# Optimization experiments

Hardware: AMD Instinct MI355X
Metric: run time of the kernel (lower is better)

## Reference

```python
import jax, jax.numpy as jnp
import numpy as np

DIM = 512
NUM_HEADS = 8
HEAD_DIM = DIM // NUM_HEADS
SCALE = HEAD_DIM ** -0.5


def setup_inputs() -> dict:
    key = jax.random.key(0)
    k1, k2, k3, k4 = jax.random.split(key, 4)
    B, C, H, W = 2, DIM, 64, 64
    x = jax.random.normal(k1, (B, C, H, W), dtype=jnp.float32)
    # torch Linear weights are [out, in]; init ~ U(-1/sqrt(in), 1/sqrt(in))
    lim = 1.0 / np.sqrt(C)
    w_qkv = jax.random.uniform(k2, (3 * C, C), minval=-lim, maxval=lim, dtype=jnp.float32)
    w_proj = jax.random.uniform(k3, (C, C), minval=-lim, maxval=lim, dtype=jnp.float32)
    b_proj = jax.random.uniform(k4, (C,), minval=-lim, maxval=lim, dtype=jnp.float32)
    return {"x": x, "w_qkv": w_qkv, "w_proj": w_proj, "b_proj": b_proj}


def reference(x, w_qkv, w_proj, b_proj):
    B, C, H, W = x.shape
    N = H * W
    h, hd = NUM_HEADS, C // NUM_HEADS
    # (B,C,H,W) -> (B,N,C)
    tokens = jnp.transpose(x, (0, 2, 3, 1)).reshape(B, N, C)
    qkv = tokens @ w_qkv.T                              # (B,N,3C)
    qkv = qkv.reshape(B, N, 3, h, hd)
    qkv = jnp.transpose(qkv, (2, 0, 3, 1, 4))           # (3,B,h,N,hd)
    q, k, v = qkv[0], qkv[1], qkv[2]
    k = k * SCALE
    # role-swapped attention: softmax over (k v^T) then apply to q
    attn = jax.nn.softmax(jnp.einsum('bhnd,bhmd->bhnm', k, v), axis=-1)  # (B,h,N,N)
    out = jnp.einsum('bhnm,bhmd->bhnd', attn, q)        # (B,h,N,hd)
    out = jnp.transpose(out, (0, 2, 1, 3)).reshape(B, H, W, C)
    # faithful to original: permute back to (B,C,H,W) THEN reshape to (B,N,C)
    out = jnp.transpose(out, (0, 3, 1, 2)).reshape(B, N, C)
    out = out @ w_proj.T + b_proj
    return out.reshape(B, C, H, W)
```

## Files before the change

kernel.cpp:

```cpp
#include <hip/hip_runtime.h>
#include <hip/hip_bf16.h>
#include <cstdint>


typedef __bf16 bf16_t;
typedef __bf16 bf16x8 __attribute__((ext_vector_type(8)));
typedef float f32x4 __attribute__((ext_vector_type(4)));
typedef unsigned int u32x4 __attribute__((ext_vector_type(4)));

#define DEVFN static __device__ __forceinline__
#define LOG2E 1.4426950408889634f

DEVFN f32x4 mfma16(bf16x8 a, bf16x8 b, f32x4 c) {
  return __builtin_amdgcn_mfma_f32_16x16x32_bf16(a, b, c, 0, 0, 0);
}
DEVFN unsigned bfbits(float x) { return (unsigned)__builtin_bit_cast(unsigned short, (bf16_t)x); }
DEVFN unsigned pack2(float lo, float hi) { return bfbits(lo) | (bfbits(hi) << 16); }

__global__ __launch_bounds__(256) void k_transpose_x(const float* __restrict__ x,
                                                     bf16_t* __restrict__ xT) {
  __shared__ bf16_t tile[64][72];
  int bid = blockIdx.x;
  int ntile = bid & 63;
  int ctile = (bid >> 6) & 7;
  int b = bid >> 9;
  int n0 = ntile << 6, c0 = ctile << 6;
  int t = threadIdx.x;
  int ci = t >> 2, nc = (t & 3) << 4;
  const float4* src4 = reinterpret_cast<const float4*>(
      x + (size_t)(b * 512 + c0 + ci) * 4096 + n0 + nc);
#pragma unroll
  for (int j4 = 0; j4 < 4; ++j4) {
    float4 v = src4[j4];
    tile[ci][nc + j4 * 4 + 0] = (bf16_t)v.x;
    tile[ci][nc + j4 * 4 + 1] = (bf16_t)v.y;
    tile[ci][nc + j4 * 4 + 2] = (bf16_t)v.z;
    tile[ci][nc + j4 * 4 + 3] = (bf16_t)v.w;
  }
  __syncthreads();
  int ni = t & 63, cc = (t >> 6) << 4;
  unsigned ob[8];
#pragma unroll
  for (int j = 0; j < 8; ++j) {
    unsigned lo = (unsigned)__builtin_bit_cast(unsigned short, tile[cc + 2 * j][ni]);
    unsigned hi = (unsigned)__builtin_bit_cast(unsigned short, tile[cc + 2 * j + 1][ni]);
    ob[j] = lo | (hi << 16);
  }
  bf16_t* dst = xT + (size_t)(b * 4096 + n0 + ni) * 512 + c0 + cc;
  reinterpret_cast<u32x4*>(dst)[0] = *(u32x4*)&ob[0];
  reinterpret_cast<u32x4*>(dst)[1] = *(u32x4*)&ob[4];
}

__global__ __launch_bounds__(256) void k_convert_w(const float* __restrict__ w,
                                                   bf16_t* __restrict__ o, int do_scale) {
  int i = (blockIdx.x * 256 + threadIdx.x) * 4;
  float4 v = *reinterpret_cast<const float4*>(w + i);
  if (do_scale) {
    const float s = 0.125f * LOG2E;
    int m = i >> 9;
    if (m >= 512 && m < 1024) { v.x *= s; v.y *= s; v.z *= s; v.w *= s; }
  }
  uint2 st; st.x = pack2(v.x, v.y); st.y = pack2(v.z, v.w);
  *reinterpret_cast<uint2*>(o + i) = st;
}

__global__ __launch_bounds__(512, 4) void k_qkv_gemm(const bf16_t* __restrict__ xT,
                                                     const bf16_t* __restrict__ wq,
                                                     bf16_t* __restrict__ Qn,
                                                     bf16_t* __restrict__ Katt,
                                                     bf16_t* __restrict__ Vbuf) {
  __shared__ bf16_t As[2][128 * 64];
  __shared__ bf16_t Bs[2][128 * 64];
  int bid = blockIdx.x;
  int tm = bid / 12, tn = bid % 12;
  int tid = threadIdx.x;
  int lane = tid & 63, wave = tid >> 6;
  int n15 = lane & 15, g = lane >> 4;
  int wm = wave & 1, wn = wave >> 1;
  int row0 = tm * 128, col0 = tn * 128;

  int srow = tid >> 3, sslot = tid & 7;
  int sgran = sslot ^ (srow & 7);
  const bf16_t* Ag = xT + (size_t)(row0 + srow) * 512 + sgran * 8;
  const bf16_t* Bg = wq + (size_t)(col0 + srow) * 512 + sgran * 8;
  int sdst = srow * 64 + sslot * 8;

  u32x4 ra0 = *reinterpret_cast<const u32x4*>(Ag);
  u32x4 ra1 = *reinterpret_cast<const u32x4*>(Ag + 64 * 512);
  u32x4 rb0 = *reinterpret_cast<const u32x4*>(Bg);
  u32x4 rb1 = *reinterpret_cast<const u32x4*>(Bg + 64 * 512);
  *reinterpret_cast<u32x4*>(&As[0][sdst]) = ra0;
  *reinterpret_cast<u32x4*>(&As[0][sdst + 4096]) = ra1;
  *reinterpret_cast<u32x4*>(&Bs[0][sdst]) = rb0;
  *reinterpret_cast<u32x4*>(&Bs[0][sdst + 4096]) = rb1;
  __syncthreads();

  f32x4 acc[4][2] = {};
  int cur = 0;
  for (int step = 0; step < 8; ++step) {
    if (step < 7) {
      int k0n = (step + 1) << 6;
      ra0 = *reinterpret_cast<const u32x4*>(Ag + k0n);
      ra1 = *reinterpret_cast<const u32x4*>(Ag + 64 * 512 + k0n);
      rb0 = *reinterpret_cast<const u32x4*>(Bg + k0n);
      rb1 = *reinterpret_cast<const u32x4*>(Bg + 64 * 512 + k0n);
    }
    const bf16_t* Al = As[cur];
    const bf16_t* Bl = Bs[cur];
#pragma unroll
    for (int kh = 0; kh < 2; ++kh) {
      bf16x8 a[4], b[2];
#pragma unroll
      for (int mf = 0; mf < 4; ++mf) {
        int r = wm * 64 + mf * 16 + n15;
        a[mf] = *reinterpret_cast<const bf16x8*>(Al + r * 64 + (((kh * 4 + g) ^ (r & 7)) << 3));
      }
#pragma unroll
      for (int nf = 0; nf < 2; ++nf) {
        int r = wn * 32 + nf * 16 + n15;
        b[nf] = *reinterpret_cast<const bf16x8*>(Bl + r * 64 + (((kh * 4 + g) ^ (r & 7)) << 3));
      }
#pragma unroll
      for (int mf = 0; mf < 4; ++mf)
#pragma unroll
        for (int nf = 0; nf < 2; ++nf) acc[mf][nf] = mfma16(a[mf], b[nf], acc[mf][nf]);
    }
    if (step < 7) {
      *reinterpret_cast<u32x4*>(&As[cur ^ 1][sdst]) = ra0;
      *reinterpret_cast<u32x4*>(&As[cur ^ 1][sdst + 4096]) = ra1;
      *reinterpret_cast<u32x4*>(&Bs[cur ^ 1][sdst]) = rb0;
      *reinterpret_cast<u32x4*>(&Bs[cur ^ 1][sdst + 4096]) = rb1;
    }
    __syncthreads();
    cur ^= 1;
  }
  int t = col0 >> 9;
  bf16_t* dstbuf = (t == 0) ? Qn : (t == 1) ? Katt : Vbuf;
#pragma unroll
  for (int mf = 0; mf < 4; ++mf)
#pragma unroll
    for (int r = 0; r < 4; ++r) {
      int rgl = row0 + wm * 64 + mf * 16 + g * 4 + r;
      int b_ = rgl >> 12, n = rgl & 4095;
#pragma unroll
      for (int nf = 0; nf < 2; ++nf) {
        int col = col0 + wn * 32 + nf * 16 + n15;
        int h = (col >> 6) & 7, d = col & 63;
        dstbuf[(((size_t)(b_ * 8 + h) * 4096 + n) << 6) + d] = (bf16_t)acc[mf][nf][r];
      }
    }
}

__global__ __launch_bounds__(256) void k_transpose_q(const bf16_t* __restrict__ Qn,
                                                     bf16_t* __restrict__ QT) {
  __shared__ bf16_t tile[64][72];
  int bid = blockIdx.x;
  int head = bid >> 6;
  int ntile = bid & 63;
  int n0 = ntile << 6;
  int t = threadIdx.x;
  int i = t >> 2, dc = (t & 3) << 4;
  const bf16_t* src = Qn + ((size_t)head * 4096 + n0 + i) * 64 + dc;
  *(u32x4*)&tile[i][dc] = reinterpret_cast<const u32x4*>(src)[0];
  *(u32x4*)&tile[i][dc + 8] = reinterpret_cast<const u32x4*>(src)[1];
  __syncthreads();
  int d = t & 63, nc2 = (t >> 6) << 4;
  unsigned ob[8];
#pragma unroll
  for (int j = 0; j < 8; ++j) {
    unsigned lo = (unsigned)__builtin_bit_cast(unsigned short, tile[nc2 + 2 * j][d]);
    unsigned hi = (unsigned)__builtin_bit_cast(unsigned short, tile[nc2 + 2 * j + 1][d]);
    ob[j] = lo | (hi << 16);
  }
  bf16_t* dst = QT + ((size_t)head * 64 + d) * 4096 + n0 + nc2;
  reinterpret_cast<u32x4*>(dst)[0] = *(u32x4*)&ob[0];
  reinterpret_cast<u32x4*>(dst)[1] = *(u32x4*)&ob[4];
}

__global__ __launch_bounds__(512, 4) void k_attn(const bf16_t* __restrict__ Katt,
                                                 const bf16_t* __restrict__ Vbuf,
                                                 const bf16_t* __restrict__ QT,
                                                 bf16_t* __restrict__ OT) {
  __shared__ bf16_t Vt[2][4096];
  __shared__ bf16_t Qs[2][4096];
  __shared__ bf16_t tlds[8][16][72];
  int bid = blockIdx.x;
  int head = bid & 15;
  int ntile = bid >> 4;
  int tid = threadIdx.x;
  int wave = tid >> 6, lane = tid & 63;
  int n15 = lane & 15, g = lane >> 4;
  int nrow0 = ntile * 128 + wave * 16;

  const bf16_t* Kp = Katt + ((size_t)head * 4096 + nrow0 + n15) * 64 + g * 8;
  bf16x8 kf0 = *reinterpret_cast<const bf16x8*>(Kp);
  bf16x8 kf1 = *reinterpret_cast<const bf16x8*>(Kp + 32);

  int vrow = tid >> 3, vg = tid & 7;
  int soff = vrow * 64 + ((vg ^ (vrow & 7)) << 3);
  const bf16_t* VgB = Vbuf + ((size_t)head * 4096 + vrow) * 64 + vg * 8;
  const bf16_t* QgB = QT + ((size_t)head * 64 + vrow) * 4096 + vg * 8;

  u32x4 vreg = *reinterpret_cast<const u32x4*>(VgB);
  u32x4 qreg = *reinterpret_cast<const u32x4*>(QgB);
  *reinterpret_cast<u32x4*>(&Vt[0][soff]) = vreg;
  *reinterpret_cast<u32x4*>(&Qs[0][soff]) = qreg;
  __syncthreads();

  f32x4 o[4] = {};
  float lacc = 0.f;
  bool hi_g = (g >= 2);
  int srcA = n15 + 16 * ((2 * g) & 3);
  int srcB = n15 + 16 * ((2 * g + 1) & 3);
  int sw = n15 & 7;
  int voff0 = n15 * 64 + (((g) ^ sw) << 3);
  int voff1 = n15 * 64 + (((g + 4) ^ sw) << 3);

  int cur = 0;
  for (int it = 0; it < 64; ++it) {
    if (it < 63) {
      vreg = *reinterpret_cast<const u32x4*>(VgB + (size_t)(it + 1) * 4096);
      qreg = *reinterpret_cast<const u32x4*>(QgB + (it + 1) * 64);
    }
    const bf16_t* Vl = Vt[cur];
    const bf16_t* Ql = Qs[cur];
    f32x4 p[4];
#pragma unroll
    for (int f = 0; f < 4; ++f) {
      bf16x8 av0 = *reinterpret_cast<const bf16x8*>(Vl + f * 1024 + voff0);
      bf16x8 av1 = *reinterpret_cast<const bf16x8*>(Vl + f * 1024 + voff1);
      f32x4 s = {};
      s = mfma16(av0, kf0, s);
      s = mfma16(av1, kf1, s);
      p[f] = s;
    }
    unsigned pk[4][2];
#pragma unroll
    for (int f = 0; f < 4; ++f) {
#pragma unroll
      for (int r = 0; r < 4; ++r) {
        float e = __builtin_amdgcn_exp2f(p[f][r]);
        p[f][r] = e;
        lacc += e;
      }
      pk[f][0] = pack2(p[f][0], p[f][1]);
      pk[f][1] = pack2(p[f][2], p[f][3]);
    }
    bf16x8 aP[2];
#pragma unroll
    for (int kk = 0; kk < 2; ++kk) {
      unsigned t00a = (unsigned)__shfl((int)pk[2 * kk + 0][0], srcA);
      unsigned t01a = (unsigned)__shfl((int)pk[2 * kk + 0][1], srcA);
      unsigned t10a = (unsigned)__shfl((int)pk[2 * kk + 1][0], srcA);
      unsigned t11a = (unsigned)__shfl((int)pk[2 * kk + 1][1], srcA);
      unsigned t00b = (unsigned)__shfl((int)pk[2 * kk + 0][0], srcB);
      unsigned t01b = (unsigned)__shfl((int)pk[2 * kk + 0][1], srcB);
      unsigned t10b = (unsigned)__shfl((int)pk[2 * kk + 1][0], srcB);
      unsigned t11b = (unsigned)__shfl((int)pk[2 * kk + 1][1], srcB);
      u32x4 uu;
      uu[0] = hi_g ? t10a : t00a;
      uu[1] = hi_g ? t11a : t01a;
      uu[2] = hi_g ? t10b : t00b;
      uu[3] = hi_g ? t11b : t01b;
      aP[kk] = __builtin_bit_cast(bf16x8, uu);
    }
#pragma unroll
    for (int db = 0; db < 4; ++db) {
      bf16x8 bq0 = *reinterpret_cast<const bf16x8*>(Ql + db * 1024 + voff0);
      bf16x8 bq1 = *reinterpret_cast<const bf16x8*>(Ql + db * 1024 + voff1);
      o[db] = mfma16(aP[0], bq0, o[db]);
      o[db] = mfma16(aP[1], bq1, o[db]);
    }
    if (it < 63) {
      *reinterpret_cast<u32x4*>(&Vt[cur ^ 1][soff]) = vreg;
      *reinterpret_cast<u32x4*>(&Qs[cur ^ 1][soff]) = qreg;
    }
    __syncthreads();
    cur ^= 1;
  }

  lacc += __shfl_xor(lacc, 16);
  lacc += __shfl_xor(lacc, 32);
#pragma unroll
  for (int r = 0; r < 4; ++r) {
    float l_r = __shfl(lacc, (g << 2) | r);
    float inv = 1.0f / l_r;
#pragma unroll
    for (int db = 0; db < 4; ++db)
      tlds[wave][g * 4 + r][n15 + 16 * db] = (bf16_t)(o[db][r] * inv);
  }
  __syncthreads();
  {
    int d = lane;
    unsigned ob[8];
#pragma unroll
    for (int j = 0; j < 8; ++j) {
      unsigned lo = (unsigned)__builtin_bit_cast(unsigned short, tlds[wave][2 * j][d]);
      unsigned hi = (unsigned)__builtin_bit_cast(unsigned short, tlds[wave][2 * j + 1][d]);
      ob[j] = lo | (hi << 16);
    }
    bf16_t* dst = OT + ((size_t)head * 64 + d) * 4096 + (size_t)ntile * 128 + wave * 16;
    reinterpret_cast<u32x4*>(dst)[0] = *(u32x4*)&ob[0];
    reinterpret_cast<u32x4*>(dst)[1] = *(u32x4*)&ob[4];
  }
}

__global__ __launch_bounds__(512, 4) void k_proj_gemm(const bf16_t* __restrict__ Y,
                                                      const bf16_t* __restrict__ wp,
                                                      const float* __restrict__ bp,
                                                      float* __restrict__ out) {
  __shared__ bf16_t As[2][128 * 64];
  __shared__ bf16_t Bs[2][128 * 64];
  int bid = blockIdx.x;
  int tm = bid >> 2, tn = bid & 3;
  int tid = threadIdx.x;
  int lane = tid & 63, wave = tid >> 6;
  int n15 = lane & 15, g = lane >> 4;
  int wm = wave & 1, wn = wave >> 1;
  int row0 = tm * 128, col0 = tn * 128;

  int srow = tid >> 3, sslot = tid & 7;
  int sgran = sslot ^ (srow & 7);
  const bf16_t* Ag = Y + (size_t)(row0 + srow) * 512 + sgran * 8;
  const bf16_t* Bg = wp + (size_t)(col0 + srow) * 512 + sgran * 8;
  int sdst = srow * 64 + sslot * 8;

  u32x4 ra0 = *reinterpret_cast<const u32x4*>(Ag);
  u32x4 ra1 = *reinterpret_cast<const u32x4*>(Ag + 64 * 512);
  u32x4 rb0 = *reinterpret_cast<const u32x4*>(Bg);
  u32x4 rb1 = *reinterpret_cast<const u32x4*>(Bg + 64 * 512);
  *reinterpret_cast<u32x4*>(&As[0][sdst]) = ra0;
  *reinterpret_cast<u32x4*>(&As[0][sdst + 4096]) = ra1;
  *reinterpret_cast<u32x4*>(&Bs[0][sdst]) = rb0;
  *reinterpret_cast<u32x4*>(&Bs[0][sdst + 4096]) = rb1;
  __syncthreads();

  f32x4 acc[4][2] = {};
  int cur = 0;
  for (int step = 0; step < 8; ++step) {
    if (step < 7) {
      int k0n = (step + 1) << 6;
      ra0 = *reinterpret_cast<const u32x4*>(Ag + k0n);
      ra1 = *reinterpret_cast<const u32x4*>(Ag + 64 * 512 + k0n);
      rb0 = *reinterpret_cast<const u32x4*>(Bg + k0n);
      rb1 = *reinterpret_cast<const u32x4*>(Bg + 64 * 512 + k0n);
    }
    const bf16_t* Al = As[cur];
    const bf16_t* Bl = Bs[cur];
#pragma unroll
    for (int kh = 0; kh < 2; ++kh) {
      bf16x8 a[4], b[2];
#pragma unroll
      for (int mf = 0; mf < 4; ++mf) {
        int r = wm * 64 + mf * 16 + n15;
        a[mf] = *reinterpret_cast<const bf16x8*>(Al + r * 64 + (((kh * 4 + g) ^ (r & 7)) << 3));
      }
#pragma unroll
      for (int nf = 0; nf < 2; ++nf) {
        int r = wn * 32 + nf * 16 + n15;
        b[nf] = *reinterpret_cast<const bf16x8*>(Bl + r * 64 + (((kh * 4 + g) ^ (r & 7)) << 3));
      }
#pragma unroll
      for (int mf = 0; mf < 4; ++mf)
#pragma unroll
        for (int nf = 0; nf < 2; ++nf) acc[mf][nf] = mfma16(a[mf], b[nf], acc[mf][nf]);
    }
    if (step < 7) {
      *reinterpret_cast<u32x4*>(&As[cur ^ 1][sdst]) = ra0;
      *reinterpret_cast<u32x4*>(&As[cur ^ 1][sdst + 4096]) = ra1;
      *reinterpret_cast<u32x4*>(&Bs[cur ^ 1][sdst]) = rb0;
      *reinterpret_cast<u32x4*>(&Bs[cur ^ 1][sdst + 4096]) = rb1;
    }
    __syncthreads();
    cur ^= 1;
  }
  float bias[2];
#pragma unroll
  for (int nf = 0; nf < 2; ++nf) bias[nf] = bp[col0 + wn * 32 + nf * 16 + n15];
#pragma unroll
  for (int mf = 0; mf < 4; ++mf)
#pragma unroll
    for (int r = 0; r < 4; ++r) {
      int rgl = row0 + wm * 64 + mf * 16 + g * 4 + r;
#pragma unroll
      for (int nf = 0; nf < 2; ++nf) {
        int col = col0 + wn * 32 + nf * 16 + n15;
        out[(size_t)rgl * 512 + col] = acc[mf][nf][r] + bias[nf];
      }
    }
}

extern "C" void kernel_launch(void* const* d_in, const int* in_sizes, int n_in,
                              void* d_out, int out_size, void* d_ws, size_t ws_size,
                              hipStream_t stream) {
  const float* x      = (const float*)d_in[0];
  const float* w_qkv  = (const float*)d_in[1];
  const float* w_proj = (const float*)d_in[2];
  const float* b_proj = (const float*)d_in[3];
  float* out = (float*)d_out;
  char* ws = (char*)d_ws;

  bf16_t* xT    = (bf16_t*)(ws + 0);
  bf16_t* wqkv  = (bf16_t*)(ws + 8388608);
  bf16_t* wproj = (bf16_t*)(ws + 9961472);
  bf16_t* Qn    = (bf16_t*)(ws + 10485760);
  bf16_t* Katt  = (bf16_t*)(ws + 18874368);
  bf16_t* Vbuf  = (bf16_t*)(ws + 27262976);
  bf16_t* QT    = (bf16_t*)(ws + 0);
  bf16_t* OT    = (bf16_t*)(ws + 10485760);

  k_transpose_x<<<dim3(1024), dim3(256), 0, stream>>>(x, xT);
  k_convert_w<<<dim3(768), dim3(256), 0, stream>>>(w_qkv, wqkv, 1);
  k_convert_w<<<dim3(256), dim3(256), 0, stream>>>(w_proj, wproj, 0);
  k_qkv_gemm<<<dim3(768), dim3(512), 0, stream>>>(xT, wqkv, Qn, Katt, Vbuf);
  k_transpose_q<<<dim3(1024), dim3(256), 0, stream>>>(Qn, QT);
  k_attn<<<dim3(512), dim3(512), 0, stream>>>(Katt, Vbuf, QT, OT);
  k_proj_gemm<<<dim3(256), dim3(512), 0, stream>>>(OT, wproj, b_proj, out);
}
```

Baseline: 239.1 us.

## Fuse Q transpose into QKV GEMM epilogue and add MFMA priority hints

The QKV GEMM now writes Q tiles already transposed (d-major, token-contiguous) by staging the accumulator through shared memory, so the separate k_transpose_q kernel and its extra round-trip through global memory are removed. The shared-memory double buffers are merged into one array so the epilogue can reuse it as a transpose tile. The attention kernel also wraps its MFMA sections in s_setprio to raise wave priority during matrix work. Workspace offsets are reshuffled so QT and OT do not alias live buffers.

Result: faster. 220.3 us (-7.9%).

```diff
diff --git a/kernel.cpp b/kernel.cpp
--- a/kernel.cpp
+++ b/kernel.cpp
@@ -66,11 +66,12 @@
 
 __global__ __launch_bounds__(512, 4) void k_qkv_gemm(const bf16_t* __restrict__ xT,
                                                      const bf16_t* __restrict__ wq,
-                                                     bf16_t* __restrict__ Qn,
+                                                     bf16_t* __restrict__ QT,
                                                      bf16_t* __restrict__ Katt,
                                                      bf16_t* __restrict__ Vbuf) {
-  __shared__ bf16_t As[2][128 * 64];
-  __shared__ bf16_t Bs[2][128 * 64];
+  __shared__ bf16_t smem[32768];
+#define AsP(b) (smem + (b) * 8192)
+#define BsP(b) (smem + 16384 + (b) * 8192)
   int bid = blockIdx.x;
   int tm = bid / 12, tn = bid % 12;
   int tid = threadIdx.x;
@@ -89,10 +90,10 @@
   u32x4 ra1 = *reinterpret_cast<const u32x4*>(Ag + 64 * 512);
   u32x4 rb0 = *reinterpret_cast<const u32x4*>(Bg);
   u32x4 rb1 = *reinterpret_cast<const u32x4*>(Bg + 64 * 512);
-  *reinterpret_cast<u32x4*>(&As[0][sdst]) = ra0;
-  *reinterpret_cast<u32x4*>(&As[0][sdst + 4096]) = ra1;
-  *reinterpret_cast<u32x4*>(&Bs[0][sdst]) = rb0;
-  *reinterpret_cast<u32x4*>(&Bs[0][sdst + 4096]) = rb1;
+  *reinterpret_cast<u32x4*>(AsP(0) + sdst) = ra0;
+  *reinterpret_cast<u32x4*>(AsP(0) + sdst + 4096) = ra1;
+  *reinterpret_cast<u32x4*>(BsP(0) + sdst) = rb0;
+  *reinterpret_cast<u32x4*>(BsP(0) + sdst + 4096) = rb1;
   __syncthreads();
 
   f32x4 acc[4][2] = {};
@@ -105,8 +106,8 @@
       rb0 = *reinterpret_cast<const u32x4*>(Bg + k0n);
       rb1 = *reinterpret_cast<const u32x4*>(Bg + 64 * 512 + k0n);
     }
-    const bf16_t* Al = As[cur];
-    const bf16_t* Bl = Bs[cur];
+    const bf16_t* Al = AsP(cur);
+    const bf16_t* Bl = BsP(cur);
 #pragma unroll
     for (int kh = 0; kh < 2; ++kh) {
       bf16x8 a[4], b[2];
@@ -126,55 +127,55 @@
         for (int nf = 0; nf < 2; ++nf) acc[mf][nf] = mfma16(a[mf], b[nf], acc[mf][nf]);
     }
     if (step < 7) {
-      *reinterpret_cast<u32x4*>(&As[cur ^ 1][sdst]) = ra0;
-      *reinterpret_cast<u32x4*>(&As[cur ^ 1][sdst + 4096]) = ra1;
-      *reinterpret_cast<u32x4*>(&Bs[cur ^ 1][sdst]) = rb0;
-      *reinterpret_cast<u32x4*>(&Bs[cur ^ 1][sdst + 4096]) = rb1;
+      *reinterpret_cast<u32x4*>(AsP(cur ^ 1) + sdst) = ra0;
+      *reinterpret_cast<u32x4*>(AsP(cur ^ 1) + sdst + 4096) = ra1;
+      *reinterpret_cast<u32x4*>(BsP(cur ^ 1) + sdst) = rb0;
+      *reinterpret_cast<u32x4*>(BsP(cur ^ 1) + sdst + 4096) = rb1;
     }
     __syncthreads();
     cur ^= 1;
   }
   int t = col0 >> 9;
-  bf16_t* dstbuf = (t == 0) ? Qn : (t == 1) ? Katt : Vbuf;
-#pragma unroll
-  for (int mf = 0; mf < 4; ++mf)
-#pragma unroll
-    for (int r = 0; r < 4; ++r) {
-      int rgl = row0 + wm * 64 + mf * 16 + g * 4 + r;
-      int b_ = rgl >> 12, n = rgl & 4095;
-#pragma unroll
-      for (int nf = 0; nf < 2; ++nf) {
-        int col = col0 + wn * 32 + nf * 16 + n15;
-        int h = (col >> 6) & 7, d = col & 63;
-        dstbuf[(((size_t)(b_ * 8 + h) * 4096 + n) << 6) + d] = (bf16_t)acc[mf][nf][r];
-      }
-    }
-}
-
-__global__ __launch_bounds__(256) void k_transpose_q(const bf16_t* __restrict__ Qn,
-                                                     bf16_t* __restrict__ QT) {
-  __shared__ bf16_t tile[64][72];
-  int bid = blockIdx.x;
-  int head = bid >> 6;
-  int ntile = bid & 63;
-  int n0 = ntile << 6;
-  int t = threadIdx.x;
-  int i = t >> 2, dc = (t & 3) << 4;
-  const bf16_t* src = Qn + ((size_t)head * 4096 + n0 + i) * 64 + dc;
-  *(u32x4*)&tile[i][dc] = reinterpret_cast<const u32x4*>(src)[0];
-  *(u32x4*)&tile[i][dc + 8] = reinterpret_cast<const u32x4*>(src)[1];
-  __syncthreads();
-  int d = t & 63, nc2 = (t >> 6) << 4;
-  unsigned ob[8];
-#pragma unroll
-  for (int j = 0; j < 8; ++j) {
-    unsigned lo = (unsigned)__builtin_bit_cast(unsigned short, tile[nc2 + 2 * j][d]);
-    unsigned hi = (unsigned)__builtin_bit_cast(unsigned short, tile[nc2 + 2 * j + 1][d]);
-    ob[j] = lo | (hi << 16);
-  }
-  bf16_t* dst = QT + ((size_t)head * 64 + d) * 4096 + n0 + nc2;
-  reinterpret_cast<u32x4*>(dst)[0] = *(u32x4*)&ob[0];
-  reinterpret_cast<u32x4*>(dst)[1] = *(u32x4*)&ob[4];
+  if (t == 0) {
+    bf16_t* T = smem;
+#pragma unroll
+    for (int mf = 0; mf < 4; ++mf)
+#pragma unroll
+      for (int r = 0; r < 4; ++r) {
+        int rl = wm * 64 + mf * 16 + g * 4 + r;
+#pragma unroll
+        for (int nf = 0; nf < 2; ++nf) {
+          int cl = wn * 32 + nf * 16 + n15;
+          T[cl * 136 + rl] = (bf16_t)acc[mf][nf][r];
+        }
+      }
+    __syncthreads();
+    int cr = tid >> 2, nch = (tid & 3) << 5;
+    int b_ = row0 >> 12, n0 = row0 & 4095;
+    int head = (col0 + cr) >> 6, d = cr & 63;
+    bf16_t* dst = QT + (((size_t)(b_ * 8 + head) * 64 + d) << 12) + n0 + nch;
+    const bf16_t* srcT = T + cr * 136 + nch;
+#pragma unroll
+    for (int j = 0; j < 4; ++j)
+      reinterpret_cast<u32x4*>(dst)[j] = *reinterpret_cast<const u32x4*>(srcT + j * 8);
+  } else {
+    bf16_t* dstbuf = (t == 1) ? Katt : Vbuf;
+#pragma unroll
+    for (int mf = 0; mf < 4; ++mf)
+#pragma unroll
+      for (int r = 0; r < 4; ++r) {
+        int rgl = row0 + wm * 64 + mf * 16 + g * 4 + r;
+        int b_ = rgl >> 12, n = rgl & 4095;
+#pragma unroll
+        for (int nf = 0; nf < 2; ++nf) {
+          int col = col0 + wn * 32 + nf * 16 + n15;
+          int h = (col >> 6) & 7, d = col & 63;
+          dstbuf[(((size_t)(b_ * 8 + h) * 4096 + n) << 6) + d] = (bf16_t)acc[mf][nf][r];
+        }
+      }
+  }
+#undef AsP
+#undef BsP
 }
 
 __global__ __launch_bounds__(512, 4) void k_attn(const bf16_t* __restrict__ Katt,
@@ -225,6 +226,7 @@
     const bf16_t* Vl = Vt[cur];
     const bf16_t* Ql = Qs[cur];
     f32x4 p[4];
+    __builtin_amdgcn_s_setprio(1);
 #pragma unroll
     for (int f = 0; f < 4; ++f) {
       bf16x8 av0 = *reinterpret_cast<const bf16x8*>(Vl + f * 1024 + voff0);
@@ -234,6 +236,7 @@
       s = mfma16(av1, kf1, s);
       p[f] = s;
     }
+    __builtin_amdgcn_s_setprio(0);
     unsigned pk[4][2];
 #pragma unroll
     for (int f = 0; f < 4; ++f) {
@@ -264,6 +267,7 @@
       uu[3] = hi_g ? t11b : t01b;
       aP[kk] = __builtin_bit_cast(bf16x8, uu);
     }
+    __builtin_amdgcn_s_setprio(1);
 #pragma unroll
     for (int db = 0; db < 4; ++db) {
       bf16x8 bq0 = *reinterpret_cast<const bf16x8*>(Ql + db * 1024 + voff0);
@@ -271,6 +275,7 @@
       o[db] = mfma16(aP[0], bq0, o[db]);
       o[db] = mfma16(aP[1], bq1, o[db]);
     }
+    __builtin_amdgcn_s_setprio(0);
     if (it < 63) {
       *reinterpret_cast<u32x4*>(&Vt[cur ^ 1][soff]) = vreg;
       *reinterpret_cast<u32x4*>(&Qs[cur ^ 1][soff]) = qreg;
@@ -403,17 +408,15 @@
   bf16_t* xT    = (bf16_t*)(ws + 0);
   bf16_t* wqkv  = (bf16_t*)(ws + 8388608);
   bf16_t* wproj = (bf16_t*)(ws + 9961472);
-  bf16_t* Qn    = (bf16_t*)(ws + 10485760);
+  bf16_t* QT    = (bf16_t*)(ws + 10485760);
   bf16_t* Katt  = (bf16_t*)(ws + 18874368);
   bf16_t* Vbuf  = (bf16_t*)(ws + 27262976);
-  bf16_t* QT    = (bf16_t*)(ws + 0);
-  bf16_t* OT    = (bf16_t*)(ws + 10485760);
+  bf16_t* OT    = (bf16_t*)(ws + 0);
 
   k_transpose_x<<<dim3(1024), dim3(256), 0, stream>>>(x, xT);
   k_convert_w<<<dim3(768), dim3(256), 0, stream>>>(w_qkv, wqkv, 1);
   k_convert_w<<<dim3(256), dim3(256), 0, stream>>>(w_proj, wproj, 0);
-  k_qkv_gemm<<<dim3(768), dim3(512), 0, stream>>>(xT, wqkv, Qn, Katt, Vbuf);
-  k_transpose_q<<<dim3(1024), dim3(256), 0, stream>>>(Qn, QT);
+  k_qkv_gemm<<<dim3(768), dim3(512), 0, stream>>>(xT, wqkv, QT, Katt, Vbuf);
   k_attn<<<dim3(512), dim3(512), 0, stream>>>(Katt, Vbuf, QT, OT);
   k_proj_gemm<<<dim3(256), dim3(512), 0, stream>>>(OT, wproj, b_proj, out);
 }
```
